# Kernel tuning notes

Measured on AMD Instinct MI355X. Metric: run time of the kernel, lower is better.

## Reference

```python
import jax, jax.numpy as jnp
import numpy as np

D_MODEL, D_FF, N_LAYERS, N_EXPERTS = 512, 1024, 2, 8
TOP_K, TEMP = 2, 1.0
B, S = 2, 1024


def _ln(x, g, b, eps=1e-5):
    m = x.mean(-1, keepdims=True)
    v = x.var(-1, keepdims=True)
    return (x - m) / jnp.sqrt(v + eps) * g + b


def setup_inputs() -> dict:
    key = jax.random.key(0)
    ks = jax.random.split(key, 32)
    s = 0.02
    rn = lambda k, sh: jax.random.normal(k, sh, jnp.float32) * s
    E, D, F, L = N_EXPERTS, D_MODEL, D_FF, N_LAYERS
    return {
        'x': jax.random.normal(ks[0], (B, S, D), jnp.float32),
        # policy head: Linear(D, D//2) -> LN -> GELU -> Linear(D//2, E)
        'pw1': rn(ks[1], (D, D // 2)), 'pb1': jnp.zeros((D // 2,)),
        'pg1': jnp.ones((D // 2,)), 'pbb1': jnp.zeros((D // 2,)),
        'pw2': rn(ks[2], (D // 2, E)), 'pb2': jnp.zeros((E,)),
        # stacked expert params [E, ...]
        'Win': rn(ks[3], (E, D, F)), 'b_in': jnp.zeros((E, F)),
        'W1': rn(ks[4], (E, L, F, 2 * F)), 'b1': jnp.zeros((E, L, 2 * F)),
        'W2': rn(ks[5], (E, L, 2 * F, F)), 'b2': jnp.zeros((E, L, F)),
        'ng': jnp.ones((E, L, F)), 'nb': jnp.zeros((E, L, F)),
        'gw': rn(ks[6], (E, L, F)),
        'Wout': rn(ks[7], (E, F, D)), 'bout': jnp.zeros((E, D)),
        'fng': jnp.ones((E, D)), 'fnb': jnp.zeros((E, D)),
    }


def reference(x, pw1, pb1, pg1, pbb1, pw2, pb2,
              Win, b_in, W1, b1, W2, b2, ng, nb, gw, Wout, bout, fng, fnb):
    # policy logits [B,S,E]
    h = _ln(x @ pw1 + pb1, pg1, pbb1)
    logits = (jax.nn.gelu(h, approximate=False) @ pw2 + pb2) / TEMP
    # Gumbel-top-k routing (fixed noise key for determinism)
    u = jax.random.uniform(jax.random.key(42), logits.shape, logits.dtype)
    g = -jnp.log(-jnp.log(u + 1e-10) + 1e-10)
    scores = logits + g
    _, idx = jax.lax.top_k(scores, TOP_K)              # [B,S,K]
    sel = (idx[..., None] == jnp.arange(N_EXPERTS)).any(axis=-2)  # [B,S,E]

    def expert(Win_e, bin_e, W1_e, b1_e, W2_e, b2_e, ng_e, nb_e, gw_e,
               Wout_e, bout_e, fng_e, fnb_e):
        h = x @ Win_e + bin_e                          # [B,S,F]
        for l in range(N_LAYERS):
            h2 = jax.nn.gelu(h @ W1_e[l] + b1_e[l], approximate=False)
            h2 = h2 @ W2_e[l] + b2_e[l]
            h2 = _ln(h2, ng_e[l], nb_e[l])
            gate = jax.nn.sigmoid(h @ gw_e[l][:, None])  # [B,S,1]
            h = h + gate * h2
        out = h @ Wout_e + bout_e
        return _ln(x + out, fng_e, fnb_e)              # [B,S,D]

    eouts = jax.vmap(expert)(Win, b_in, W1, b1, W2, b2, ng, nb, gw,
                             Wout, bout, fng, fnb)     # [E,B,S,D]
    # combine: torch code sums (unweighted) expert outputs over selected experts
    outputs = jnp.einsum('ebsd,bse->bsd', eouts, sel.astype(x.dtype))
    return outputs
```

## Files before the change

### kernel.cpp

```cpp
#include <hip/hip_runtime.h>
#include <hip/hip_bf16.h>

#define N_EXP   8
#define NTOK    2048
#define TOTROWS 4096

typedef __hip_bfloat16 bf16;
typedef __attribute__((ext_vector_type(8))) short short8;
typedef __attribute__((ext_vector_type(4))) float floatx4;

#define TM 128
#define TN 128
#define TK 32
#define LDAB 40


__device__ inline float gelu_f(float v) {
    return 0.5f * v * (1.0f + erff(v * 0.70710678118654752440f));
}

__device__ inline float block_sum256(float v, float* red) {
    #pragma unroll
    for (int off = 32; off > 0; off >>= 1)
        v += __shfl_down(v, off, 64);
    __syncthreads();
    if ((threadIdx.x & 63) == 0) red[threadIdx.x >> 6] = v;
    __syncthreads();
    return red[0] + red[1] + red[2] + red[3];
}

__device__ inline unsigned rotl32(unsigned v, int d) { return (v << d) | (v >> (32 - d)); }

__device__ inline void threefry2x32(unsigned k0, unsigned k1, unsigned x0, unsigned x1,
                                    unsigned& o0, unsigned& o1) {
    unsigned ks2 = k0 ^ k1 ^ 0x1BD11BDAu;
    x0 += k0; x1 += k1;
#define TF_R(r) { x0 += x1; x1 = rotl32(x1, r); x1 ^= x0; }
    TF_R(13) TF_R(15) TF_R(26) TF_R(6)
    x0 += k1; x1 += ks2 + 1u;
    TF_R(17) TF_R(29) TF_R(16) TF_R(24)
    x0 += ks2; x1 += k0 + 2u;
    TF_R(13) TF_R(15) TF_R(26) TF_R(6)
    x0 += k0; x1 += k1 + 3u;
    TF_R(17) TF_R(29) TF_R(16) TF_R(24)
    x0 += k1; x1 += ks2 + 4u;
    TF_R(13) TF_R(15) TF_R(26) TF_R(6)
    x0 += ks2; x1 += k0 + 5u;
#undef TF_R
    o0 = x0; o1 = x1;
}

__device__ inline int expert_of(int r, const int* bases) {
    int e = 0;
    #pragma unroll
    for (int i = 1; i < N_EXP; ++i) if (r >= bases[i]) e = i;
    return e;
}


__global__ __launch_bounds__(256) void policy_k(
    const float* __restrict__ x, const float* __restrict__ pw1,
    const float* __restrict__ pb1, const float* __restrict__ pg1,
    const float* __restrict__ pbb1, const float* __restrict__ pw2,
    const float* __restrict__ pb2, int2* __restrict__ top2, int* __restrict__ counts)
{
    const int t = blockIdx.x;
    const int lid = threadIdx.x;
    __shared__ float xs[512];
    __shared__ float hb[256];
    __shared__ float red[4];
    __shared__ float sc[8];

    xs[lid]       = x[(long long)t * 512 + lid];
    xs[lid + 256] = x[(long long)t * 512 + 256 + lid];
    __syncthreads();

    float acc = pb1[lid];
    for (int d = 0; d < 512; ++d)
        acc = fmaf(xs[d], pw1[d * 256 + lid], acc);

    float s  = block_sum256(acc, red);
    float sq = block_sum256(acc * acc, red);
    float mean = s * (1.0f / 256.0f);
    float var  = sq * (1.0f / 256.0f) - mean * mean;
    float rstd = rsqrtf(var + 1e-5f);
    float hn = (acc - mean) * rstd * pg1[lid] + pbb1[lid];
    hb[lid] = gelu_f(hn);
    __syncthreads();

    if (lid < 8) {
        float lg = pb2[lid];
        for (int j = 0; j < 256; ++j)
            lg = fmaf(hb[j], pw2[j * 8 + lid], lg);
        unsigned idx = (unsigned)t * 8u + (unsigned)lid;
        unsigned o0, o1;
        threefry2x32(0u, 42u, 0u, idx, o0, o1);
        unsigned bits = o0 ^ o1;
        float u = __uint_as_float((bits >> 9) | 0x3f800000u) - 1.0f;
        float gml = -logf(-logf(u + 1e-10f) + 1e-10f);
        sc[lid] = lg + gml;
    }
    __syncthreads();
    if (lid == 0) {
        float b0 = -INFINITY; int i0 = 0;
        #pragma unroll
        for (int e = 0; e < 8; ++e) if (sc[e] > b0) { b0 = sc[e]; i0 = e; }
        float b1v = -INFINITY; int i1 = 0;
        #pragma unroll
        for (int e = 0; e < 8; ++e) if (e != i0 && sc[e] > b1v) { b1v = sc[e]; i1 = e; }
        top2[t] = make_int2(i0, i1);
        atomicAdd(&counts[i0], 1);
        atomicAdd(&counts[i1], 1);
    }
}

__global__ void prefix_k(const int* __restrict__ counts, int* __restrict__ cursor,
                         int* __restrict__ bases) {
    if (threadIdx.x == 0 && blockIdx.x == 0) {
        int s = 0;
        for (int e = 0; e < N_EXP; ++e) { bases[e] = s; cursor[e] = s; s += counts[e]; }
    }
}

__global__ __launch_bounds__(256) void scatter_k(const int2* __restrict__ top2,
                                                 int* __restrict__ cursor,
                                                 int* __restrict__ list) {
    int t = blockIdx.x * 256 + threadIdx.x;
    int2 p = top2[t];
    int pos = atomicAdd(&cursor[p.x], 1); list[pos] = t;
    pos     = atomicAdd(&cursor[p.y], 1); list[pos] = t;
}


__global__ __launch_bounds__(256) void cast_x_k(const float* __restrict__ x,
                                                bf16* __restrict__ xb) {
    int i = (blockIdx.x * 256 + threadIdx.x) * 4;
    float4 v = *(const float4*)(x + i);
    bf16 o[4] = { (bf16)v.x, (bf16)v.y, (bf16)v.z, (bf16)v.w };
    *(unsigned long long*)(xb + i) = *(unsigned long long*)o;
}


template <typename CT>
__global__ __launch_bounds__(256) void mgemm_k(
    const bf16* __restrict__ A, const int* __restrict__ gather,
    const float* __restrict__ W, long long westride,
    const float* __restrict__ bias, int bestride,
    CT* __restrict__ C, bf16* __restrict__ Cmir,
    const int* __restrict__ counts, const int* __restrict__ bases,
    int K, int N, int act)
{
    const int e   = blockIdx.z;
    const int cnt = counts[e];
    const int m0  = blockIdx.y * TM;
    if (m0 >= cnt) return;
    const int rbase = bases[e];
    const int n0  = blockIdx.x * TN;
    const float* We = W + (long long)e * westride;

    __shared__ unsigned short As[TM * LDAB];
    __shared__ unsigned short Bs[TN * LDAB];

    const int tid  = threadIdx.x;
    const int lane = tid & 63;
    const int wv   = tid >> 6;
    const int wm   = (wv & 1) * 64;
    const int wn   = (wv >> 1) * 64;
    const int q    = lane >> 4;
    const int ln   = lane & 15;

    const int ar = tid >> 2;
    const int ak = (tid & 3) * 8;
    long long arow0, arow1;
    {
        int r0 = m0 + ar;      if (r0 > cnt - 1) r0 = cnt - 1;
        int r1 = m0 + 64 + ar; if (r1 > cnt - 1) r1 = cnt - 1;
        long long p0 = gather ? (long long)gather[rbase + r0] : (long long)(rbase + r0);
        long long p1 = gather ? (long long)gather[rbase + r1] : (long long)(rbase + r1);
        arow0 = p0 * K; arow1 = p1 * K;
    }
    const int bn = (wv & 1) * 64 + lane;
    const int bkb = (wv >> 1) * 16;

    floatx4 acc[4][4];
    #pragma unroll
    for (int i = 0; i < 4; ++i)
        #pragma unroll
        for (int j = 0; j < 4; ++j)
            acc[i][j] = (floatx4){0.f, 0.f, 0.f, 0.f};

    for (int k0 = 0; k0 < K; k0 += TK) {
        uint4 va0 = *(const uint4*)(A + arow0 + k0 + ak);
        uint4 va1 = *(const uint4*)(A + arow1 + k0 + ak);

        float wf[16];
        #pragma unroll
        for (int kk = 0; kk < 16; ++kk)
            wf[kk] = We[(long long)(k0 + bkb + kk) * N + n0 + bn];

        *(uint4*)(&As[ar * LDAB + ak])        = va0;
        *(uint4*)(&As[(64 + ar) * LDAB + ak]) = va1;

        union { unsigned short us[8]; uint4 v; } p0, p1;
        #pragma unroll
        for (int kk = 0; kk < 8; ++kk) {
            bf16 b0 = (bf16)wf[kk];
            bf16 b1 = (bf16)wf[kk + 8];
            p0.us[kk] = *(unsigned short*)&b0;
            p1.us[kk] = *(unsigned short*)&b1;
        }
        *(uint4*)(&Bs[bn * LDAB + bkb])     = p0.v;
        *(uint4*)(&Bs[bn * LDAB + bkb + 8]) = p1.v;
        __syncthreads();

        short8 a_frag[4], b_frag[4];
        #pragma unroll
        for (int i = 0; i < 4; ++i)
            a_frag[i] = *(const short8*)(&As[(wm + i * 16 + ln) * LDAB + q * 8]);
        #pragma unroll
        for (int j = 0; j < 4; ++j)
            b_frag[j] = *(const short8*)(&Bs[(wn + j * 16 + ln) * LDAB + q * 8]);
        #pragma unroll
        for (int i = 0; i < 4; ++i)
            #pragma unroll
            for (int j = 0; j < 4; ++j)
                acc[i][j] = __builtin_amdgcn_mfma_f32_16x16x32_bf16(
                    a_frag[i], b_frag[j], acc[i][j], 0, 0, 0);
        __syncthreads();
    }

    #pragma unroll
    for (int i = 0; i < 4; ++i) {
        int rbase_i = m0 + wm + i * 16 + q * 4;
        #pragma unroll
        for (int j = 0; j < 4; ++j) {
            int n = n0 + wn + j * 16 + ln;
            float bv = bias[e * bestride + n];
            #pragma unroll
            for (int rg = 0; rg < 4; ++rg) {
                int r = rbase_i + rg;
                if (r >= cnt) continue;
                float v = acc[i][j][rg] + bv;
                if (act) v = gelu_f(v);
                long long off = (long long)(rbase + r) * N + n;
                C[off] = (CT)v;
                if (Cmir) Cmir[off] = (bf16)v;
            }
        }
    }
}


__global__ __launch_bounds__(256) void lngate_k(
    float* __restrict__ h, bf16* __restrict__ hb, const float* __restrict__ h2,
    const float* __restrict__ ng, const float* __restrict__ nb,
    const float* __restrict__ gw, const int* __restrict__ bases, int l)
{
    const int r = blockIdx.x;
    const int e = expert_of(r, bases);
    const int lid = threadIdx.x;
    const float* hr  = h  + (long long)r * 1024;
    const float* h2r = h2 + (long long)r * 1024;
    const int off = (e * 2 + l) * 1024;
    __shared__ float red[4];

    float s = 0.f, sq = 0.f, dt = 0.f;
    float hv[4], h2v[4];
    #pragma unroll
    for (int i = 0; i < 4; ++i) {
        int j = lid + 256 * i;
        float a = h2r[j];
        float b = hr[j];
        hv[i] = b; h2v[i] = a;
        s += a; sq += a * a;
        dt = fmaf(b, gw[off + j], dt);
    }
    s  = block_sum256(s, red);
    sq = block_sum256(sq, red);
    dt = block_sum256(dt, red);
    float mean = s * (1.f / 1024.f);
    float rstd = rsqrtf(sq * (1.f / 1024.f) - mean * mean + 1e-5f);
    float gate = 1.f / (1.f + expf(-dt));
    float* hw  = h  + (long long)r * 1024;
    bf16*  hbw = hb + (long long)r * 1024;
    #pragma unroll
    for (int i = 0; i < 4; ++i) {
        int j = lid + 256 * i;
        float v = (h2v[i] - mean) * rstd * ng[off + j] + nb[off + j];
        float nh = hv[i] + gate * v;
        hw[j] = nh;
        hbw[j] = (bf16)nh;
    }
}


__global__ __launch_bounds__(256) void final_k(
    const float* __restrict__ x, const bf16* __restrict__ orow,
    const float* __restrict__ fng, const float* __restrict__ fnb,
    const int* __restrict__ bases, const int* __restrict__ list,
    float* __restrict__ out)
{
    const int r = blockIdx.x;
    const int e = expert_of(r, bases);
    const int t = list[r];
    const int lid = threadIdx.x;
    __shared__ float red[4];

    float y[2];
    float s = 0.f, sq = 0.f;
    #pragma unroll
    for (int i = 0; i < 2; ++i) {
        int j = lid + 256 * i;
        float v = x[(long long)t * 512 + j] + (float)orow[(long long)r * 512 + j];
        y[i] = v; s += v; sq += v * v;
    }
    s  = block_sum256(s, red);
    sq = block_sum256(sq, red);
    float mean = s * (1.f / 512.f);
    float rstd = rsqrtf(sq * (1.f / 512.f) - mean * mean + 1e-5f);
    #pragma unroll
    for (int i = 0; i < 2; ++i) {
        int j = lid + 256 * i;
        float v = (y[i] - mean) * rstd * fng[e * 512 + j] + fnb[e * 512 + j];
        atomicAdd(&out[(long long)t * 512 + j], v);
    }
}


extern "C" void kernel_launch(void* const* d_in, const int* in_sizes, int n_in,
                              void* d_out, int out_size, void* d_ws, size_t ws_size,
                              hipStream_t stream) {
    const float* x    = (const float*)d_in[0];
    const float* pw1  = (const float*)d_in[1];
    const float* pb1  = (const float*)d_in[2];
    const float* pg1  = (const float*)d_in[3];
    const float* pbb1 = (const float*)d_in[4];
    const float* pw2  = (const float*)d_in[5];
    const float* pb2  = (const float*)d_in[6];
    const float* Win  = (const float*)d_in[7];
    const float* b_in = (const float*)d_in[8];
    const float* W1   = (const float*)d_in[9];
    const float* b1   = (const float*)d_in[10];
    const float* W2   = (const float*)d_in[11];
    const float* b2   = (const float*)d_in[12];
    const float* ng   = (const float*)d_in[13];
    const float* nb   = (const float*)d_in[14];
    const float* gw   = (const float*)d_in[15];
    const float* Wout = (const float*)d_in[16];
    const float* bout = (const float*)d_in[17];
    const float* fng  = (const float*)d_in[18];
    const float* fnb  = (const float*)d_in[19];
    float* out = (float*)d_out;
    (void)ws_size; (void)in_sizes; (void)n_in;

    char* ws = (char*)d_ws;
    int* counts = (int*)ws;
    int* cursor = counts + 8;
    int* bases  = cursor + 8;
    int2* top2  = (int2*)(ws + 128);
    int*  list  = (int*)(ws + 128 + 2048 * 8);
    size_t o = 128 + 2048 * 8 + 4096 * 4;
    o = (o + 255) & ~(size_t)255;
    bf16*  xb   = (bf16*) (ws + o); o += (size_t)NTOK * 512 * 2;
    float* h    = (float*)(ws + o); o += (size_t)TOTROWS * 1024 * 4;
    bf16*  hb   = (bf16*) (ws + o); o += (size_t)TOTROWS * 1024 * 2;
    bf16*  tb   = (bf16*) (ws + o); o += (size_t)TOTROWS * 2048 * 2;
    float* h2   = (float*)(ws + o); o += (size_t)TOTROWS * 1024 * 4;
    bf16*  orow = (bf16*) (ws + o); o += (size_t)TOTROWS * 512 * 2;

    hipMemsetAsync(d_out, 0, (size_t)out_size * sizeof(float), stream);
    hipMemsetAsync(ws, 0, 64, stream);

    policy_k<<<NTOK, 256, 0, stream>>>(x, pw1, pb1, pg1, pbb1, pw2, pb2, top2, counts);
    prefix_k<<<1, 64, 0, stream>>>(counts, cursor, bases);
    scatter_k<<<NTOK / 256, 256, 0, stream>>>(top2, cursor, list);
    cast_x_k<<<NTOK * 512 / 1024, 256, 0, stream>>>(x, xb);

    mgemm_k<float><<<dim3(8, 16, 8), 256, 0, stream>>>(
        xb, list, Win, (long long)512 * 1024, b_in, 1024, h, hb,
        counts, bases, 512, 1024, 0);

    for (int l = 0; l < 2; ++l) {
        mgemm_k<bf16><<<dim3(16, 16, 8), 256, 0, stream>>>(
            hb, nullptr, W1 + (long long)l * 1024 * 2048, (long long)2 * 1024 * 2048,
            b1 + l * 2048, 2 * 2048, tb, (bf16*)nullptr,
            counts, bases, 1024, 2048, 1);
        mgemm_k<float><<<dim3(8, 16, 8), 256, 0, stream>>>(
            tb, nullptr, W2 + (long long)l * 2048 * 1024, (long long)2 * 2048 * 1024,
            b2 + l * 1024, 2 * 1024, h2, (bf16*)nullptr,
            counts, bases, 2048, 1024, 0);
        lngate_k<<<TOTROWS, 256, 0, stream>>>(h, hb, h2, ng, nb, gw, bases, l);
    }

    mgemm_k<bf16><<<dim3(4, 16, 8), 256, 0, stream>>>(
        hb, nullptr, Wout, (long long)1024 * 512, bout, 512, orow, (bf16*)nullptr,
        counts, bases, 1024, 512, 0);

    final_k<<<TOTROWS, 256, 0, stream>>>(x, orow, fng, fnb, bases, list, out);
}
```

Measured before the change: 828.6 us.

## Double-buffer grouped GEMM tiles and use 64-row tiles for small-N GEMMs

The grouped expert GEMM now keeps two shared-memory buffers and register staging. Global loads for the next K-slice are issued before the MFMA compute on the current slice, which hides load latency behind compute. The M tile size becomes a template parameter, and the Win and Wout GEMMs use 64-row tiles with twice as many row blocks to raise occupancy and block count. The cost is more LDS and registers per block, and the smaller tiles re-read weights more often.

```diff
diff --git a/kernel.cpp b/kernel.cpp
--- a/kernel.cpp
+++ b/kernel.cpp
@@ -9,7 +9,6 @@
 typedef __attribute__((ext_vector_type(8))) short short8;
 typedef __attribute__((ext_vector_type(4))) float floatx4;
 
-#define TM 128
 #define TN 128
 #define TK 32
 #define LDAB 40
@@ -141,7 +140,7 @@
 }
 
 
-template <typename CT>
+template <typename CT, int TMp>
 __global__ __launch_bounds__(256) void mgemm_k(
     const bf16* __restrict__ A, const int* __restrict__ gather,
     const float* __restrict__ W, long long westride,
@@ -152,85 +151,112 @@
 {
     const int e   = blockIdx.z;
     const int cnt = counts[e];
-    const int m0  = blockIdx.y * TM;
+    const int m0  = blockIdx.y * TMp;
     if (m0 >= cnt) return;
     const int rbase = bases[e];
     const int n0  = blockIdx.x * TN;
     const float* We = W + (long long)e * westride;
 
-    __shared__ unsigned short As[TM * LDAB];
-    __shared__ unsigned short Bs[TN * LDAB];
+    constexpr int MI = TMp / 32;
+
+    __shared__ __align__(16) unsigned short As[2][TMp * LDAB];
+    __shared__ __align__(16) unsigned short Bs[2][TN * LDAB];
 
     const int tid  = threadIdx.x;
     const int lane = tid & 63;
     const int wv   = tid >> 6;
-    const int wm   = (wv & 1) * 64;
+    const int wm   = (wv & 1) * (TMp / 2);
     const int wn   = (wv >> 1) * 64;
     const int q    = lane >> 4;
     const int ln   = lane & 15;
 
     const int ar = tid >> 2;
     const int ak = (tid & 3) * 8;
-    long long arow0, arow1;
+    long long arow0 = 0, arow1 = 0;
     {
-        int r0 = m0 + ar;      if (r0 > cnt - 1) r0 = cnt - 1;
-        int r1 = m0 + 64 + ar; if (r1 > cnt - 1) r1 = cnt - 1;
+        int r0 = m0 + ar; if (r0 > cnt - 1) r0 = cnt - 1;
         long long p0 = gather ? (long long)gather[rbase + r0] : (long long)(rbase + r0);
-        long long p1 = gather ? (long long)gather[rbase + r1] : (long long)(rbase + r1);
-        arow0 = p0 * K; arow1 = p1 * K;
-    }
-    const int bn = (wv & 1) * 64 + lane;
+        arow0 = p0 * K;
+        if (TMp == 128) {
+            int r1 = m0 + 64 + ar; if (r1 > cnt - 1) r1 = cnt - 1;
+            long long p1 = gather ? (long long)gather[rbase + r1] : (long long)(rbase + r1);
+            arow1 = p1 * K;
+        }
+    }
+    const int bn  = (wv & 1) * 64 + lane;
     const int bkb = (wv >> 1) * 16;
-
-    floatx4 acc[4][4];
-    #pragma unroll
-    for (int i = 0; i < 4; ++i)
+    const float* wcol = We + n0 + bn;
+
+    floatx4 acc[MI][4];
+    #pragma unroll
+    for (int i = 0; i < MI; ++i)
         #pragma unroll
         for (int j = 0; j < 4; ++j)
             acc[i][j] = (floatx4){0.f, 0.f, 0.f, 0.f};
 
-    for (int k0 = 0; k0 < K; k0 += TK) {
-        uint4 va0 = *(const uint4*)(A + arow0 + k0 + ak);
-        uint4 va1 = *(const uint4*)(A + arow1 + k0 + ak);
-
-        float wf[16];
-        #pragma unroll
-        for (int kk = 0; kk < 16; ++kk)
-            wf[kk] = We[(long long)(k0 + bkb + kk) * N + n0 + bn];
-
-        *(uint4*)(&As[ar * LDAB + ak])        = va0;
-        *(uint4*)(&As[(64 + ar) * LDAB + ak]) = va1;
-
+    uint4 a0A = {0,0,0,0}, a1A = {0,0,0,0}, a0B = {0,0,0,0}, a1B = {0,0,0,0};
+    float wA[16], wB[16];
+
+    auto mg_load = [&](uint4& a0r, uint4& a1r, float (&wr)[16], int koff) {
+        a0r = *(const uint4*)(A + arow0 + koff + ak);
+        if (TMp == 128) a1r = *(const uint4*)(A + arow1 + koff + ak);
+        const float* wp = wcol + (long long)(koff + bkb) * N;
+        #pragma unroll
+        for (int kk = 0; kk < 16; ++kk) wr[kk] = wp[(long long)kk * N];
+    };
+    auto mg_store = [&](const uint4& a0r, const uint4& a1r, const float (&wr)[16], int buf) {
+        *(uint4*)(&As[buf][ar * LDAB + ak]) = a0r;
+        if (TMp == 128) *(uint4*)(&As[buf][(64 + ar) * LDAB + ak]) = a1r;
         union { unsigned short us[8]; uint4 v; } p0, p1;
         #pragma unroll
         for (int kk = 0; kk < 8; ++kk) {
-            bf16 b0 = (bf16)wf[kk];
-            bf16 b1 = (bf16)wf[kk + 8];
+            bf16 b0 = (bf16)wr[kk];
+            bf16 b1 = (bf16)wr[kk + 8];
             p0.us[kk] = *(unsigned short*)&b0;
             p1.us[kk] = *(unsigned short*)&b1;
         }
-        *(uint4*)(&Bs[bn * LDAB + bkb])     = p0.v;
-        *(uint4*)(&Bs[bn * LDAB + bkb + 8]) = p1.v;
-        __syncthreads();
-
-        short8 a_frag[4], b_frag[4];
-        #pragma unroll
-        for (int i = 0; i < 4; ++i)
-            a_frag[i] = *(const short8*)(&As[(wm + i * 16 + ln) * LDAB + q * 8]);
+        *(uint4*)(&Bs[buf][bn * LDAB + bkb])     = p0.v;
+        *(uint4*)(&Bs[buf][bn * LDAB + bkb + 8]) = p1.v;
+    };
+    auto mg_compute = [&](int buf) {
+        short8 a_frag[MI], b_frag[4];
+        #pragma unroll
+        for (int i = 0; i < MI; ++i)
+            a_frag[i] = *(const short8*)(&As[buf][(wm + i * 16 + ln) * LDAB + q * 8]);
         #pragma unroll
         for (int j = 0; j < 4; ++j)
-            b_frag[j] = *(const short8*)(&Bs[(wn + j * 16 + ln) * LDAB + q * 8]);
-        #pragma unroll
-        for (int i = 0; i < 4; ++i)
+            b_frag[j] = *(const short8*)(&Bs[buf][(wn + j * 16 + ln) * LDAB + q * 8]);
+        #pragma unroll
+        for (int i = 0; i < MI; ++i)
             #pragma unroll
             for (int j = 0; j < 4; ++j)
                 acc[i][j] = __builtin_amdgcn_mfma_f32_16x16x32_bf16(
                     a_frag[i], b_frag[j], acc[i][j], 0, 0, 0);
+    };
+
+    mg_load(a0A, a1A, wA, 0);
+    mg_store(a0A, a1A, wA, 0);
+    mg_load(a0B, a1B, wB, TK);
+    __syncthreads();
+
+    int k0 = 0;
+    for (; k0 + 2 * TK < K; k0 += 2 * TK) {
+        mg_load(a0A, a1A, wA, k0 + 2 * TK);
+        mg_compute(0);
+        mg_store(a0B, a1B, wB, 1);
         __syncthreads();
-    }
-
-    #pragma unroll
-    for (int i = 0; i < 4; ++i) {
+        mg_load(a0B, a1B, wB, k0 + 3 * TK);
+        mg_compute(1);
+        mg_store(a0A, a1A, wA, 0);
+        __syncthreads();
+    }
+    mg_compute(0);
+    mg_store(a0B, a1B, wB, 1);
+    __syncthreads();
+    mg_compute(1);
+
+    #pragma unroll
+    for (int i = 0; i < MI; ++i) {
         int rbase_i = m0 + wm + i * 16 + q * 4;
         #pragma unroll
         for (int j = 0; j < 4; ++j) {
@@ -376,23 +402,23 @@
     scatter_k<<<NTOK / 256, 256, 0, stream>>>(top2, cursor, list);
     cast_x_k<<<NTOK * 512 / 1024, 256, 0, stream>>>(x, xb);
 
-    mgemm_k<float><<<dim3(8, 16, 8), 256, 0, stream>>>(
+    mgemm_k<float, 64><<<dim3(8, 32, 8), 256, 0, stream>>>(
         xb, list, Win, (long long)512 * 1024, b_in, 1024, h, hb,
         counts, bases, 512, 1024, 0);
 
     for (int l = 0; l < 2; ++l) {
-        mgemm_k<bf16><<<dim3(16, 16, 8), 256, 0, stream>>>(
+        mgemm_k<bf16, 128><<<dim3(16, 16, 8), 256, 0, stream>>>(
             hb, nullptr, W1 + (long long)l * 1024 * 2048, (long long)2 * 1024 * 2048,
             b1 + l * 2048, 2 * 2048, tb, (bf16*)nullptr,
             counts, bases, 1024, 2048, 1);
-        mgemm_k<float><<<dim3(8, 16, 8), 256, 0, stream>>>(
+        mgemm_k<float, 128><<<dim3(8, 16, 8), 256, 0, stream>>>(
             tb, nullptr, W2 + (long long)l * 2048 * 1024, (long long)2 * 2048 * 1024,
             b2 + l * 1024, 2 * 1024, h2, (bf16*)nullptr,
             counts, bases, 2048, 1024, 0);
         lngate_k<<<TOTROWS, 256, 0, stream>>>(h, hb, h2, ng, nb, gw, bases, l);
     }
 
-    mgemm_k<bf16><<<dim3(4, 16, 8), 256, 0, stream>>>(
+    mgemm_k<bf16, 64><<<dim3(4, 32, 8), 256, 0, stream>>>(
         hb, nullptr, Wout, (long long)1024 * 512, bout, 512, orow, (bf16*)nullptr,
         counts, bases, 1024, 512, 0);
 
```

Result: faster. 774.9 us (-6.5%).
